# Optimization experiments

Measured on AMD Instinct MI355X. Metric: run time of the kernel, lower is better.

The kernel has to match this reference:

```python
import jax, jax.numpy as jnp
import numpy as np

N, L, D, H = 16384, 10, 256, 2
DH = D // H


def setup_inputs() -> dict:
    key = jax.random.key(0)
    ks = jax.random.split(key, 8)
    messages = jax.random.normal(ks[0], (N, L, D), dtype=jnp.float32)
    timestamps = jnp.sort(jax.random.uniform(ks[1], (N, L), dtype=jnp.float32) * 1000.0, axis=-1)
    # TGN-style time encoder params: w initialized as 1/10^linspace(0,9,D)
    w_time = (1.0 / (10.0 ** jnp.linspace(0.0, 9.0, D))).astype(jnp.float32)
    b_time = jnp.zeros((D,), dtype=jnp.float32)
    w_in = jax.random.normal(ks[2], (3 * D, D), dtype=jnp.float32) * 0.02
    b_in = jnp.zeros((3 * D,), dtype=jnp.float32)
    w_out = jax.random.normal(ks[3], (D, D), dtype=jnp.float32) * 0.02
    b_out = jnp.zeros((D,), dtype=jnp.float32)
    lengths = jax.random.randint(ks[4], (N,), 0, L, dtype=jnp.int32)  # valid = lengths+1 in [1, L]
    return {"messages": messages, "timestamps": timestamps, "w_time": w_time,
            "b_time": b_time, "w_in": w_in, "b_in": b_in, "w_out": w_out,
            "b_out": b_out, "lengths": lengths}


def _attn_aggregate(messages, timestamps, w_time, b_time, w_in, b_in, w_out, b_out, lengths):
    # time deltas relative to most recent message per node (as in the torch loop)
    deltas = timestamps - timestamps[:, -1:]                       # [N, L]
    te = jnp.cos(deltas[..., None] * w_time + b_time)              # [N, L, D] time embeddings

    wq, wk, wv = w_in[:D], w_in[D:2 * D], w_in[2 * D:]
    bq, bk, bv = b_in[:D], b_in[D:2 * D], b_in[2 * D:]
    # query = messages, key = time embeddings, value = messages (MHA over per-node window)
    q = (messages @ wq.T + bq).reshape(N, L, H, DH)
    k = (te @ wk.T + bk).reshape(N, L, H, DH)
    v = (messages @ wv.T + bv).reshape(N, L, H, DH)

    scores = jnp.einsum("nqhd,nkhd->nhqk", q, k) / jnp.sqrt(jnp.float32(DH))  # [N,H,L,L]
    # right-aligned padding: first (L - (lengths+1)) positions are padding
    valid = lengths + 1                                            # [N], in [1, L]
    pos = jnp.arange(L)
    pad = pos[None, :] < (L - valid)[:, None]                      # [N, L] True = pad
    scores = jnp.where(pad[:, None, None, :], jnp.float32(-1e9), scores)
    attn = jax.nn.softmax(scores, axis=-1)
    ctx = jnp.einsum("nhqk,nkhd->nqhd", attn, v).reshape(N, L, D)
    out = ctx @ w_out.T + b_out                                    # [N, L, D]
    return out[:, -1, :]                                           # aggregated message per node [N, D]


def reference(messages, timestamps, w_time, b_time, w_in, b_in, w_out, b_out, lengths):
    return _attn_aggregate(messages, timestamps, w_time, b_time, w_in, b_in, w_out, b_out, lengths)
```

## Files before the change

### kernel.cpp

```cpp
#include <hip/hip_runtime.h>
#include <hip/hip_bf16.h>

#define N_S 16384
#define LL 10
#define DD 256

typedef __bf16 bf16;
typedef __attribute__((ext_vector_type(8))) __bf16 bf16x8_t;
typedef __attribute__((ext_vector_type(4))) __bf16 bf16x4_t;
typedef __attribute__((ext_vector_type(4))) float f32x4_t;

__device__ __forceinline__ float fast_cos(float x) {
    float r = x * 0.15915494309189535f;
    r = r - rintf(r);
    return __builtin_amdgcn_cosf(r);
}

__device__ __forceinline__ float bf2f(unsigned short u) {
    return __uint_as_float((unsigned)u << 16);
}

__global__ __launch_bounds__(256) void k_pre(
    const float* __restrict__ w_in, const float* __restrict__ b_in,
    const float* __restrict__ w_out, const float* __restrict__ b_out,
    bf16* __restrict__ Apk, bf16* __restrict__ Cpk,
    float* __restrict__ u, float* __restrict__ p,
    float* __restrict__ c2, float* __restrict__ dvec)
{
    const int bid = blockIdx.x;
    const int tid = threadIdx.x;
    if (bid < 512) {
        const int g = bid * 256 + tid;
        {
            const int kk = g >> 9;
            const int nn = g & 511;
            const int h = nn >> 8;
            const int j = nn & 255;
            const float* wq = w_in + (size_t)(h * 128) * 256;
            const float* wk = w_in + (size_t)(256 + h * 128) * 256;
            float s = 0.f;
            for (int d = 0; d < 128; ++d)
                s += wq[d * 256 + kk] * wk[d * 256 + j];
            const int lane = (((kk & 31) >> 3) << 4) + (nn & 15);
            const int idx = ((((nn >> 4) * 8 + (kk >> 5)) * 64 + lane) << 3) + (kk & 7);
            Apk[idx] = (bf16)s;
        }
        {
            const int oo = g >> 9;
            const int kk2 = g & 511;
            const int h = kk2 >> 8;
            const int i = kk2 & 255;
            const float* wv = w_in + (size_t)(512 + h * 128) * 256;
            float s = 0.f;
            for (int d = 0; d < 128; ++d)
                s += wv[d * 256 + i] * w_out[oo * 256 + h * 128 + d];
            const int lane = (((kk2 & 31) >> 3) << 4) + (oo & 15);
            const int idx = ((((oo >> 4) * 16 + (kk2 >> 5)) * 64 + lane) << 3) + (kk2 & 7);
            Cpk[idx] = (bf16)s;
        }
    } else {
        for (int j = tid; j < 512; j += 256) {
            const int h = j >> 8; const int jj = j & 255;
            float s = 0.f;
            for (int d = 0; d < 128; ++d)
                s += b_in[h * 128 + d] * w_in[(size_t)(256 + h * 128 + d) * 256 + jj];
            u[j] = s;
        }
        for (int i = tid; i < 512; i += 256) {
            const int h = i >> 8; const int ii = i & 255;
            float s = 0.f;
            for (int d = 0; d < 128; ++d)
                s += w_in[(size_t)(h * 128 + d) * 256 + ii] * b_in[256 + h * 128 + d];
            p[i] = s;
        }
        if (tid < 2) {
            float s = 0.f;
            for (int d = 0; d < 128; ++d)
                s += b_in[tid * 128 + d] * b_in[256 + tid * 128 + d];
            c2[tid] = s;
        }
        if (tid < 256) {
            float s = b_out[tid];
            for (int t = 0; t < 256; ++t)
                s += b_in[512 + t] * w_out[tid * 256 + t];
            dvec[tid] = s;
        }
    }
}

__global__ __launch_bounds__(256) void k_gemm1(
    const float* __restrict__ messages, const bf16* __restrict__ Apk,
    const float* __restrict__ u, bf16* __restrict__ G)
{
    const int lane = threadIdx.x & 63;
    const int wid = threadIdx.x >> 6;
    const int mblk = blockIdx.x;
    const int nblk = blockIdx.y;
    const int m0 = mblk * 128 + wid * 32;
    const int r16 = lane & 15;
    const int q4 = lane >> 4;

    f32x4_t acc[2][4];
    #pragma unroll
    for (int a = 0; a < 2; ++a)
        #pragma unroll
        for (int b = 0; b < 4; ++b)
            acc[a][b] = (f32x4_t)(0.f);

    #pragma unroll
    for (int ks = 0; ks < 8; ++ks) {
        bf16x8_t afr[2];
        #pragma unroll
        for (int mt = 0; mt < 2; ++mt) {
            const int row = m0 + mt * 16 + r16;
            const float* src = messages + (size_t)row * (LL * DD) + (LL - 1) * DD + ks * 32 + q4 * 8;
            f32x4_t lo = *(const f32x4_t*)(src);
            f32x4_t hi = *(const f32x4_t*)(src + 4);
            bf16x8_t a;
            a[0] = (bf16)lo[0]; a[1] = (bf16)lo[1]; a[2] = (bf16)lo[2]; a[3] = (bf16)lo[3];
            a[4] = (bf16)hi[0]; a[5] = (bf16)hi[1]; a[6] = (bf16)hi[2]; a[7] = (bf16)hi[3];
            afr[mt] = a;
        }
        #pragma unroll
        for (int nt = 0; nt < 4; ++nt) {
            const int nblk16 = nblk * 4 + nt;
            bf16x8_t b = *(const bf16x8_t*)(Apk + (((size_t)(nblk16 * 8 + ks) * 64 + lane) << 3));
            #pragma unroll
            for (int mt = 0; mt < 2; ++mt)
                acc[mt][nt] = __builtin_amdgcn_mfma_f32_16x16x32_bf16(afr[mt], b, acc[mt][nt], 0, 0, 0);
        }
    }
    #pragma unroll
    for (int mt = 0; mt < 2; ++mt)
        #pragma unroll
        for (int nt = 0; nt < 4; ++nt) {
            const int col = nblk * 64 + nt * 16 + r16;
            const float ub = u[col];
            #pragma unroll
            for (int r = 0; r < 4; ++r) {
                const int row = m0 + mt * 16 + q4 * 4 + r;
                G[(size_t)row * 512 + col] = (bf16)(acc[mt][nt][r] + ub);
            }
        }
}

__global__ __launch_bounds__(256) void k_attn(
    const float* __restrict__ messages, const float* __restrict__ timestamps,
    const float* __restrict__ w_time, const float* __restrict__ b_time,
    const int* __restrict__ lengths, const float* __restrict__ p,
    const float* __restrict__ c2, bf16* __restrict__ GY)
{
    const int lane = threadIdx.x & 63;
    const int wid = threadIdx.x >> 6;
    const int n = blockIdx.x * 4 + wid;
    const int d0 = lane * 4;

    const unsigned short* Grow = (const unsigned short*)(GY + (size_t)n * 512);
    float g0[4], g1[4];
    {
        ushort4 a = *(const ushort4*)(Grow + d0);
        ushort4 b = *(const ushort4*)(Grow + 256 + d0);
        g0[0] = bf2f(a.x); g0[1] = bf2f(a.y); g0[2] = bf2f(a.z); g0[3] = bf2f(a.w);
        g1[0] = bf2f(b.x); g1[1] = bf2f(b.y); g1[2] = bf2f(b.z); g1[3] = bf2f(b.w);
    }

    float wt[4], bt[4], m9[4];
    *(f32x4_t*)wt = *(const f32x4_t*)(w_time + d0);
    *(f32x4_t*)bt = *(const f32x4_t*)(b_time + d0);
    *(f32x4_t*)m9 = *(const f32x4_t*)(messages + (size_t)n * (LL * DD) + (LL - 1) * DD + d0);

    const float* tsrow = timestamps + n * LL;
    const float tlast = tsrow[LL - 1];
    const int valid = lengths[n] + 1;
    const int lmin = LL - valid;

    float s0a, s0b;
    {
        f32x4_t p0 = *(const f32x4_t*)(p + d0);
        f32x4_t p1 = *(const f32x4_t*)(p + 256 + d0);
        s0a = m9[0] * p0[0] + m9[1] * p0[1] + m9[2] * p0[2] + m9[3] * p0[3];
        s0b = m9[0] * p1[0] + m9[1] * p1[1] + m9[2] * p1[2] + m9[3] * p1[3];
        #pragma unroll
        for (int m = 1; m < 64; m <<= 1) {
            s0a += __shfl_xor(s0a, m);
            s0b += __shfl_xor(s0b, m);
        }
        s0a += c2[0];
        s0b += c2[1];
    }

    const float scale = 0.08838834764831845f;
    float sc0[LL], sc1[LL];
    #pragma unroll
    for (int l = 0; l < LL; ++l) {
        if (l >= lmin) {
            const float delta = tsrow[l] - tlast;
            float pa = 0.f, pb = 0.f;
            #pragma unroll
            for (int j = 0; j < 4; ++j) {
                const float te = fast_cos(delta * wt[j] + bt[j]);
                pa += g0[j] * te;
                pb += g1[j] * te;
            }
            #pragma unroll
            for (int m = 1; m < 64; m <<= 1) {
                pa += __shfl_xor(pa, m);
                pb += __shfl_xor(pb, m);
            }
            sc0[l] = (pa + s0a) * scale;
            sc1[l] = (pb + s0b) * scale;
        } else {
            sc0[l] = -1e30f;
            sc1[l] = -1e30f;
        }
    }

    float mx0 = sc0[0], mx1 = sc1[0];
    #pragma unroll
    for (int l = 1; l < LL; ++l) {
        mx0 = fmaxf(mx0, sc0[l]);
        mx1 = fmaxf(mx1, sc1[l]);
    }
    float w0[LL], w1[LL];
    float den0 = 0.f, den1 = 0.f;
    #pragma unroll
    for (int l = 0; l < LL; ++l) {
        w0[l] = (l >= lmin) ? __expf(sc0[l] - mx0) : 0.f;
        w1[l] = (l >= lmin) ? __expf(sc1[l] - mx1) : 0.f;
        den0 += w0[l];
        den1 += w1[l];
    }
    const float inv0 = 1.f / den0, inv1 = 1.f / den1;

    float y0[4] = {0.f, 0.f, 0.f, 0.f}, y1[4] = {0.f, 0.f, 0.f, 0.f};
    #pragma unroll
    for (int l = 0; l < LL; ++l) {
        if (l >= lmin) {
            float mv[4];
            if (l == LL - 1) {
                mv[0] = m9[0]; mv[1] = m9[1]; mv[2] = m9[2]; mv[3] = m9[3];
            } else {
                *(f32x4_t*)mv = *(const f32x4_t*)(messages + (size_t)n * (LL * DD) + l * DD + d0);
            }
            const float a0 = w0[l] * inv0, a1 = w1[l] * inv1;
            #pragma unroll
            for (int j = 0; j < 4; ++j) {
                y0[j] += a0 * mv[j];
                y1[j] += a1 * mv[j];
            }
        }
    }

    bf16x4_t v0, v1;
    v0[0] = (bf16)y0[0]; v0[1] = (bf16)y0[1]; v0[2] = (bf16)y0[2]; v0[3] = (bf16)y0[3];
    v1[0] = (bf16)y1[0]; v1[1] = (bf16)y1[1]; v1[2] = (bf16)y1[2]; v1[3] = (bf16)y1[3];
    *(bf16x4_t*)(GY + (size_t)n * 512 + d0) = v0;
    *(bf16x4_t*)(GY + (size_t)n * 512 + 256 + d0) = v1;
}

__global__ __launch_bounds__(256) void k_gemm2(
    const bf16* __restrict__ Y, const bf16* __restrict__ Cpk,
    const float* __restrict__ dvec, float* __restrict__ out)
{
    const int lane = threadIdx.x & 63;
    const int wid = threadIdx.x >> 6;
    const int mblk = blockIdx.x;
    const int nblk = blockIdx.y;
    const int m0 = mblk * 128 + wid * 32;
    const int r16 = lane & 15;
    const int q4 = lane >> 4;

    f32x4_t acc[2][4];
    #pragma unroll
    for (int a = 0; a < 2; ++a)
        #pragma unroll
        for (int b = 0; b < 4; ++b)
            acc[a][b] = (f32x4_t)(0.f);

    #pragma unroll
    for (int ks = 0; ks < 16; ++ks) {
        bf16x8_t afr[2];
        #pragma unroll
        for (int mt = 0; mt < 2; ++mt) {
            const int row = m0 + mt * 16 + r16;
            afr[mt] = *(const bf16x8_t*)(Y + (size_t)row * 512 + ks * 32 + q4 * 8);
        }
        #pragma unroll
        for (int nt = 0; nt < 4; ++nt) {
            const int nblk16 = nblk * 4 + nt;
            bf16x8_t b = *(const bf16x8_t*)(Cpk + (((size_t)(nblk16 * 16 + ks) * 64 + lane) << 3));
            #pragma unroll
            for (int mt = 0; mt < 2; ++mt)
                acc[mt][nt] = __builtin_amdgcn_mfma_f32_16x16x32_bf16(afr[mt], b, acc[mt][nt], 0, 0, 0);
        }
    }
    #pragma unroll
    for (int mt = 0; mt < 2; ++mt)
        #pragma unroll
        for (int nt = 0; nt < 4; ++nt) {
            const int col = nblk * 64 + nt * 16 + r16;
            const float db = dvec[col];
            #pragma unroll
            for (int r = 0; r < 4; ++r) {
                const int row = m0 + mt * 16 + q4 * 4 + r;
                out[(size_t)row * 256 + col] = acc[mt][nt][r] + db;
            }
        }
}

extern "C" void kernel_launch(void* const* d_in, const int* in_sizes, int n_in,
                              void* d_out, int out_size, void* d_ws, size_t ws_size,
                              hipStream_t stream) {
    const float* messages   = (const float*)d_in[0];
    const float* timestamps = (const float*)d_in[1];
    const float* w_time     = (const float*)d_in[2];
    const float* b_time     = (const float*)d_in[3];
    const float* w_in       = (const float*)d_in[4];
    const float* b_in       = (const float*)d_in[5];
    const float* w_out      = (const float*)d_in[6];
    const float* b_out      = (const float*)d_in[7];
    const int*   lengths    = (const int*)d_in[8];
    float* out = (float*)d_out;

    char* ws = (char*)d_ws;
    bf16*  Apk  = (bf16*)(ws);
    bf16*  Cpk  = (bf16*)(ws + 262144);
    float* u    = (float*)(ws + 524288);
    float* p    = (float*)(ws + 526336);
    float* c2   = (float*)(ws + 528384);
    float* dvec = (float*)(ws + 528448);
    bf16*  GY   = (bf16*)(ws + 1048576);

    k_pre<<<dim3(513), dim3(256), 0, stream>>>(w_in, b_in, w_out, b_out,
                                               Apk, Cpk, u, p, c2, dvec);
    k_gemm1<<<dim3(128, 8), dim3(256), 0, stream>>>(messages, Apk, u, GY);
    k_attn<<<dim3(4096), dim3(256), 0, stream>>>(messages, timestamps, w_time, b_time,
                                                 lengths, p, c2, GY);
    k_gemm2<<<dim3(128, 4), dim3(256), 0, stream>>>(GY, Cpk, dvec, out);
}
```

Measured before the change: 326.4 us.

## Fuse gemm1, attention and gemm2 into one kernel with LDS staging

Merges the three per-node kernels into one kernel that processes 32 nodes per block. The intermediate G/Y rows stay in shared memory instead of round-tripping through global memory, and two launches go away. The precompute kernel is also split into 1025 blocks so the Apk and Cpk products run in separate blocks, with unrolled inner loops. The trade-off is a grid of only 512 blocks and heavier per-wave register use (16 accumulators), which may reduce occupancy and latency hiding.

```diff
diff --git a/kernel.cpp b/kernel.cpp
--- a/kernel.cpp
+++ b/kernel.cpp
@@ -14,10 +14,6 @@
     float r = x * 0.15915494309189535f;
     r = r - rintf(r);
     return __builtin_amdgcn_cosf(r);
-}
-
-__device__ __forceinline__ float bf2f(unsigned short u) {
-    return __uint_as_float((unsigned)u << 16);
 }
 
 __global__ __launch_bounds__(256) void k_pre(
@@ -31,37 +27,38 @@
     const int tid = threadIdx.x;
     if (bid < 512) {
         const int g = bid * 256 + tid;
-        {
-            const int kk = g >> 9;
-            const int nn = g & 511;
-            const int h = nn >> 8;
-            const int j = nn & 255;
-            const float* wq = w_in + (size_t)(h * 128) * 256;
-            const float* wk = w_in + (size_t)(256 + h * 128) * 256;
-            float s = 0.f;
-            for (int d = 0; d < 128; ++d)
-                s += wq[d * 256 + kk] * wk[d * 256 + j];
-            const int lane = (((kk & 31) >> 3) << 4) + (nn & 15);
-            const int idx = ((((nn >> 4) * 8 + (kk >> 5)) * 64 + lane) << 3) + (kk & 7);
-            Apk[idx] = (bf16)s;
-        }
-        {
-            const int oo = g >> 9;
-            const int kk2 = g & 511;
-            const int h = kk2 >> 8;
-            const int i = kk2 & 255;
-            const float* wv = w_in + (size_t)(512 + h * 128) * 256;
-            float s = 0.f;
-            for (int d = 0; d < 128; ++d)
-                s += wv[d * 256 + i] * w_out[oo * 256 + h * 128 + d];
-            const int lane = (((kk2 & 31) >> 3) << 4) + (oo & 15);
-            const int idx = ((((oo >> 4) * 16 + (kk2 >> 5)) * 64 + lane) << 3) + (kk2 & 7);
-            Cpk[idx] = (bf16)s;
-        }
+        const int kk = g >> 9;
+        const int nn = g & 511;
+        const int h = nn >> 8;
+        const int j = nn & 255;
+        const float* wq = w_in + (size_t)(h * 128) * 256;
+        const float* wk = w_in + (size_t)(256 + h * 128) * 256;
+        float s = 0.f;
+        #pragma unroll 16
+        for (int d = 0; d < 128; ++d)
+            s += wq[d * 256 + kk] * wk[d * 256 + j];
+        const int lane = (((kk & 31) >> 3) << 4) + (nn & 15);
+        const int idx = ((((nn >> 4) * 8 + (kk >> 5)) * 64 + lane) << 3) + (kk & 7);
+        Apk[idx] = (bf16)s;
+    } else if (bid < 1024) {
+        const int g = (bid - 512) * 256 + tid;
+        const int oo = g >> 9;
+        const int kk2 = g & 511;
+        const int h = kk2 >> 8;
+        const int i = kk2 & 255;
+        const float* wv = w_in + (size_t)(512 + h * 128) * 256;
+        float s = 0.f;
+        #pragma unroll 16
+        for (int d = 0; d < 128; ++d)
+            s += wv[d * 256 + i] * w_out[oo * 256 + h * 128 + d];
+        const int lane = (((kk2 & 31) >> 3) << 4) + (oo & 15);
+        const int idx = ((((oo >> 4) * 16 + (kk2 >> 5)) * 64 + lane) << 3) + (kk2 & 7);
+        Cpk[idx] = (bf16)s;
     } else {
         for (int j = tid; j < 512; j += 256) {
             const int h = j >> 8; const int jj = j & 255;
             float s = 0.f;
+            #pragma unroll 16
             for (int d = 0; d < 128; ++d)
                 s += b_in[h * 128 + d] * w_in[(size_t)(256 + h * 128 + d) * 256 + jj];
             u[j] = s;
@@ -69,18 +66,21 @@
         for (int i = tid; i < 512; i += 256) {
             const int h = i >> 8; const int ii = i & 255;
             float s = 0.f;
+            #pragma unroll 16
             for (int d = 0; d < 128; ++d)
                 s += w_in[(size_t)(h * 128 + d) * 256 + ii] * b_in[256 + h * 128 + d];
             p[i] = s;
         }
         if (tid < 2) {
             float s = 0.f;
+            #pragma unroll 16
             for (int d = 0; d < 128; ++d)
                 s += b_in[tid * 128 + d] * b_in[256 + tid * 128 + d];
             c2[tid] = s;
         }
         if (tid < 256) {
             float s = b_out[tid];
+            #pragma unroll 16
             for (int t = 0; t < 256; ++t)
                 s += b_in[512 + t] * w_out[tid * 256 + t];
             dvec[tid] = s;
@@ -88,224 +88,195 @@
     }
 }
 
-__global__ __launch_bounds__(256) void k_gemm1(
-    const float* __restrict__ messages, const bf16* __restrict__ Apk,
-    const float* __restrict__ u, bf16* __restrict__ G)
+__global__ __launch_bounds__(256, 4) void k_fused(
+    const float* __restrict__ messages, const float* __restrict__ timestamps,
+    const float* __restrict__ w_time, const float* __restrict__ b_time,
+    const int* __restrict__ lengths,
+    const bf16* __restrict__ Apk, const bf16* __restrict__ Cpk,
+    const float* __restrict__ u, const float* __restrict__ p,
+    const float* __restrict__ c2, const float* __restrict__ dvec,
+    float* __restrict__ out)
 {
-    const int lane = threadIdx.x & 63;
-    const int wid = threadIdx.x >> 6;
-    const int mblk = blockIdx.x;
-    const int nblk = blockIdx.y;
-    const int m0 = mblk * 128 + wid * 32;
+    __shared__ __align__(16) bf16 Gs[32][520];
+
+    const int tid = threadIdx.x;
+    const int lane = tid & 63;
+    const int wid = tid >> 6;
     const int r16 = lane & 15;
     const int q4 = lane >> 4;
-
-    f32x4_t acc[2][4];
-    #pragma unroll
-    for (int a = 0; a < 2; ++a)
-        #pragma unroll
-        for (int b = 0; b < 4; ++b)
-            acc[a][b] = (f32x4_t)(0.f);
-
-    #pragma unroll
-    for (int ks = 0; ks < 8; ++ks) {
-        bf16x8_t afr[2];
-        #pragma unroll
-        for (int mt = 0; mt < 2; ++mt) {
-            const int row = m0 + mt * 16 + r16;
-            const float* src = messages + (size_t)row * (LL * DD) + (LL - 1) * DD + ks * 32 + q4 * 8;
-            f32x4_t lo = *(const f32x4_t*)(src);
-            f32x4_t hi = *(const f32x4_t*)(src + 4);
+    const int n0 = blockIdx.x * 32;
+
+    {
+        const int wr = wid >> 1;
+        const int wc = wid & 1;
+        f32x4_t acc[16];
+        #pragma unroll
+        for (int nt = 0; nt < 16; ++nt) acc[nt] = (f32x4_t)(0.f);
+
+        const int arow = n0 + wr * 16 + r16;
+        const float* abase = messages + (size_t)arow * (LL * DD) + (LL - 1) * DD + q4 * 8;
+        #pragma unroll
+        for (int ks = 0; ks < 8; ++ks) {
+            f32x4_t lo = *(const f32x4_t*)(abase + ks * 32);
+            f32x4_t hi = *(const f32x4_t*)(abase + ks * 32 + 4);
             bf16x8_t a;
             a[0] = (bf16)lo[0]; a[1] = (bf16)lo[1]; a[2] = (bf16)lo[2]; a[3] = (bf16)lo[3];
             a[4] = (bf16)hi[0]; a[5] = (bf16)hi[1]; a[6] = (bf16)hi[2]; a[7] = (bf16)hi[3];
-            afr[mt] = a;
-        }
-        #pragma unroll
-        for (int nt = 0; nt < 4; ++nt) {
-            const int nblk16 = nblk * 4 + nt;
-            bf16x8_t b = *(const bf16x8_t*)(Apk + (((size_t)(nblk16 * 8 + ks) * 64 + lane) << 3));
-            #pragma unroll
-            for (int mt = 0; mt < 2; ++mt)
-                acc[mt][nt] = __builtin_amdgcn_mfma_f32_16x16x32_bf16(afr[mt], b, acc[mt][nt], 0, 0, 0);
+            #pragma unroll
+            for (int nt = 0; nt < 16; ++nt) {
+                const int nblk16 = wc * 16 + nt;
+                bf16x8_t b = *(const bf16x8_t*)(Apk + (((size_t)(nblk16 * 8 + ks) * 64 + lane) << 3));
+                acc[nt] = __builtin_amdgcn_mfma_f32_16x16x32_bf16(a, b, acc[nt], 0, 0, 0);
+            }
+        }
+        #pragma unroll
+        for (int nt = 0; nt < 16; ++nt) {
+            const int col = wc * 256 + nt * 16 + r16;
+            const float ub = u[col];
+            #pragma unroll
+            for (int r = 0; r < 4; ++r)
+                Gs[wr * 16 + q4 * 4 + r][col] = (bf16)(acc[nt][r] + ub);
         }
     }
-    #pragma unroll
-    for (int mt = 0; mt < 2; ++mt)
-        #pragma unroll
-        for (int nt = 0; nt < 4; ++nt) {
-            const int col = nblk * 64 + nt * 16 + r16;
-            const float ub = u[col];
+    __syncthreads();
+
+    {
+        const int d0 = lane * 4;
+        float wt[4], bt[4], pv0[4], pv1[4];
+        *(f32x4_t*)wt = *(const f32x4_t*)(w_time + d0);
+        *(f32x4_t*)bt = *(const f32x4_t*)(b_time + d0);
+        *(f32x4_t*)pv0 = *(const f32x4_t*)(p + d0);
+        *(f32x4_t*)pv1 = *(const f32x4_t*)(p + 256 + d0);
+        const float c20 = c2[0], c21 = c2[1];
+        const float scale = 0.08838834764831845f;
+
+        #pragma unroll
+        for (int i = 0; i < 8; ++i) {
+            const int s = wid * 8 + i;
+            const int n = n0 + s;
+
+            float g0[4], g1[4];
+            {
+                bf16x4_t ga = *(const bf16x4_t*)(&Gs[s][d0]);
+                bf16x4_t gb = *(const bf16x4_t*)(&Gs[s][256 + d0]);
+                #pragma unroll
+                for (int j = 0; j < 4; ++j) { g0[j] = (float)ga[j]; g1[j] = (float)gb[j]; }
+            }
+            float m9[4];
+            *(f32x4_t*)m9 = *(const f32x4_t*)(messages + (size_t)n * (LL * DD) + (LL - 1) * DD + d0);
+
+            const float* tsrow = timestamps + n * LL;
+            const float tlast = tsrow[LL - 1];
+            const int valid = lengths[n] + 1;
+            const int lmin = LL - valid;
+
+            float s0a = m9[0]*pv0[0] + m9[1]*pv0[1] + m9[2]*pv0[2] + m9[3]*pv0[3];
+            float s0b = m9[0]*pv1[0] + m9[1]*pv1[1] + m9[2]*pv1[2] + m9[3]*pv1[3];
+            #pragma unroll
+            for (int m = 1; m < 64; m <<= 1) {
+                s0a += __shfl_xor(s0a, m);
+                s0b += __shfl_xor(s0b, m);
+            }
+            s0a += c20; s0b += c21;
+
+            float sc0[LL], sc1[LL];
+            #pragma unroll
+            for (int l = 0; l < LL; ++l) {
+                if (l >= lmin) {
+                    const float delta = tsrow[l] - tlast;
+                    float pa = 0.f, pb = 0.f;
+                    #pragma unroll
+                    for (int j = 0; j < 4; ++j) {
+                        const float te = fast_cos(delta * wt[j] + bt[j]);
+                        pa += g0[j] * te;
+                        pb += g1[j] * te;
+                    }
+                    #pragma unroll
+                    for (int m = 1; m < 64; m <<= 1) {
+                        pa += __shfl_xor(pa, m);
+                        pb += __shfl_xor(pb, m);
+                    }
+                    sc0[l] = (pa + s0a) * scale;
+                    sc1[l] = (pb + s0b) * scale;
+                } else {
+                    sc0[l] = -1e30f;
+                    sc1[l] = -1e30f;
+                }
+            }
+
+            float mx0 = sc0[0], mx1 = sc1[0];
+            #pragma unroll
+            for (int l = 1; l < LL; ++l) {
+                mx0 = fmaxf(mx0, sc0[l]);
+                mx1 = fmaxf(mx1, sc1[l]);
+            }
+            float w0[LL], w1[LL];
+            float den0 = 0.f, den1 = 0.f;
+            #pragma unroll
+            for (int l = 0; l < LL; ++l) {
+                w0[l] = (l >= lmin) ? __expf(sc0[l] - mx0) : 0.f;
+                w1[l] = (l >= lmin) ? __expf(sc1[l] - mx1) : 0.f;
+                den0 += w0[l];
+                den1 += w1[l];
+            }
+            const float inv0 = 1.f / den0, inv1 = 1.f / den1;
+
+            float y0[4] = {0.f,0.f,0.f,0.f}, y1[4] = {0.f,0.f,0.f,0.f};
+            #pragma unroll
+            for (int l = 0; l < LL; ++l) {
+                if (l >= lmin) {
+                    float mv[4];
+                    if (l == LL - 1) {
+                        mv[0]=m9[0]; mv[1]=m9[1]; mv[2]=m9[2]; mv[3]=m9[3];
+                    } else {
+                        *(f32x4_t*)mv = *(const f32x4_t*)(messages + (size_t)n * (LL * DD) + l * DD + d0);
+                    }
+                    const float a0 = w0[l] * inv0, a1 = w1[l] * inv1;
+                    #pragma unroll
+                    for (int j = 0; j < 4; ++j) {
+                        y0[j] += a0 * mv[j];
+                        y1[j] += a1 * mv[j];
+                    }
+                }
+            }
+
+            bf16x4_t v0, v1;
+            v0[0]=(bf16)y0[0]; v0[1]=(bf16)y0[1]; v0[2]=(bf16)y0[2]; v0[3]=(bf16)y0[3];
+            v1[0]=(bf16)y1[0]; v1[1]=(bf16)y1[1]; v1[2]=(bf16)y1[2]; v1[3]=(bf16)y1[3];
+            *(bf16x4_t*)(&Gs[s][d0]) = v0;
+            *(bf16x4_t*)(&Gs[s][256 + d0]) = v1;
+        }
+    }
+    __syncthreads();
+
+    {
+        const int wr2 = wid >> 1;
+        const int wc2 = wid & 1;
+        f32x4_t acc2[8];
+        #pragma unroll
+        for (int nt = 0; nt < 8; ++nt) acc2[nt] = (f32x4_t)(0.f);
+
+        #pragma unroll
+        for (int ks = 0; ks < 16; ++ks) {
+            bf16x8_t a = *(const bf16x8_t*)(&Gs[wr2 * 16 + r16][ks * 32 + q4 * 8]);
+            #pragma unroll
+            for (int nt = 0; nt < 8; ++nt) {
+                const int nblk16 = wc2 * 8 + nt;
+                bf16x8_t b = *(const bf16x8_t*)(Cpk + (((size_t)(nblk16 * 16 + ks) * 64 + lane) << 3));
+                acc2[nt] = __builtin_amdgcn_mfma_f32_16x16x32_bf16(a, b, acc2[nt], 0, 0, 0);
+            }
+        }
+        #pragma unroll
+        for (int nt = 0; nt < 8; ++nt) {
+            const int col = wc2 * 128 + nt * 16 + r16;
+            const float db = dvec[col];
             #pragma unroll
             for (int r = 0; r < 4; ++r) {
-                const int row = m0 + mt * 16 + q4 * 4 + r;
-                G[(size_t)row * 512 + col] = (bf16)(acc[mt][nt][r] + ub);
-            }
-        }
-}
-
-__global__ __launch_bounds__(256) void k_attn(
-    const float* __restrict__ messages, const float* __restrict__ timestamps,
-    const float* __restrict__ w_time, const float* __restrict__ b_time,
-    const int* __restrict__ lengths, const float* __restrict__ p,
-    const float* __restrict__ c2, bf16* __restrict__ GY)
-{
-    const int lane = threadIdx.x & 63;
-    const int wid = threadIdx.x >> 6;
-    const int n = blockIdx.x * 4 + wid;
-    const int d0 = lane * 4;
-
-    const unsigned short* Grow = (const unsigned short*)(GY + (size_t)n * 512);
-    float g0[4], g1[4];
-    {
-        ushort4 a = *(const ushort4*)(Grow + d0);
-        ushort4 b = *(const ushort4*)(Grow + 256 + d0);
-        g0[0] = bf2f(a.x); g0[1] = bf2f(a.y); g0[2] = bf2f(a.z); g0[3] = bf2f(a.w);
-        g1[0] = bf2f(b.x); g1[1] = bf2f(b.y); g1[2] = bf2f(b.z); g1[3] = bf2f(b.w);
+                const int row = n0 + wr2 * 16 + q4 * 4 + r;
+                out[(size_t)row * 256 + col] = acc2[nt][r] + db;
+            }
+        }
     }
-
-    float wt[4], bt[4], m9[4];
-    *(f32x4_t*)wt = *(const f32x4_t*)(w_time + d0);
-    *(f32x4_t*)bt = *(const f32x4_t*)(b_time + d0);
-    *(f32x4_t*)m9 = *(const f32x4_t*)(messages + (size_t)n * (LL * DD) + (LL - 1) * DD + d0);
-
-    const float* tsrow = timestamps + n * LL;
-    const float tlast = tsrow[LL - 1];
-    const int valid = lengths[n] + 1;
-    const int lmin = LL - valid;
-
-    float s0a, s0b;
-    {
-        f32x4_t p0 = *(const f32x4_t*)(p + d0);
-        f32x4_t p1 = *(const f32x4_t*)(p + 256 + d0);
-        s0a = m9[0] * p0[0] + m9[1] * p0[1] + m9[2] * p0[2] + m9[3] * p0[3];
-        s0b = m9[0] * p1[0] + m9[1] * p1[1] + m9[2] * p1[2] + m9[3] * p1[3];
-        #pragma unroll
-        for (int m = 1; m < 64; m <<= 1) {
-            s0a += __shfl_xor(s0a, m);
-            s0b += __shfl_xor(s0b, m);
-        }
-        s0a += c2[0];
-        s0b += c2[1];
-    }
-
-    const float scale = 0.08838834764831845f;
-    float sc0[LL], sc1[LL];
-    #pragma unroll
-    for (int l = 0; l < LL; ++l) {
-        if (l >= lmin) {
-            const float delta = tsrow[l] - tlast;
-            float pa = 0.f, pb = 0.f;
-            #pragma unroll
-            for (int j = 0; j < 4; ++j) {
-                const float te = fast_cos(delta * wt[j] + bt[j]);
-                pa += g0[j] * te;
-                pb += g1[j] * te;
-            }
-            #pragma unroll
-            for (int m = 1; m < 64; m <<= 1) {
-                pa += __shfl_xor(pa, m);
-                pb += __shfl_xor(pb, m);
-            }
-            sc0[l] = (pa + s0a) * scale;
-            sc1[l] = (pb + s0b) * scale;
-        } else {
-            sc0[l] = -1e30f;
-            sc1[l] = -1e30f;
-        }
-    }
-
-    float mx0 = sc0[0], mx1 = sc1[0];
-    #pragma unroll
-    for (int l = 1; l < LL; ++l) {
-        mx0 = fmaxf(mx0, sc0[l]);
-        mx1 = fmaxf(mx1, sc1[l]);
-    }
-    float w0[LL], w1[LL];
-    float den0 = 0.f, den1 = 0.f;
-    #pragma unroll
-    for (int l = 0; l < LL; ++l) {
-        w0[l] = (l >= lmin) ? __expf(sc0[l] - mx0) : 0.f;
-        w1[l] = (l >= lmin) ? __expf(sc1[l] - mx1) : 0.f;
-        den0 += w0[l];
-        den1 += w1[l];
-    }
-    const float inv0 = 1.f / den0, inv1 = 1.f / den1;
-
-    float y0[4] = {0.f, 0.f, 0.f, 0.f}, y1[4] = {0.f, 0.f, 0.f, 0.f};
-    #pragma unroll
-    for (int l = 0; l < LL; ++l) {
-        if (l >= lmin) {
-            float mv[4];
-            if (l == LL - 1) {
-                mv[0] = m9[0]; mv[1] = m9[1]; mv[2] = m9[2]; mv[3] = m9[3];
-            } else {
-                *(f32x4_t*)mv = *(const f32x4_t*)(messages + (size_t)n * (LL * DD) + l * DD + d0);
-            }
-            const float a0 = w0[l] * inv0, a1 = w1[l] * inv1;
-            #pragma unroll
-            for (int j = 0; j < 4; ++j) {
-                y0[j] += a0 * mv[j];
-                y1[j] += a1 * mv[j];
-            }
-        }
-    }
-
-    bf16x4_t v0, v1;
-    v0[0] = (bf16)y0[0]; v0[1] = (bf16)y0[1]; v0[2] = (bf16)y0[2]; v0[3] = (bf16)y0[3];
-    v1[0] = (bf16)y1[0]; v1[1] = (bf16)y1[1]; v1[2] = (bf16)y1[2]; v1[3] = (bf16)y1[3];
-    *(bf16x4_t*)(GY + (size_t)n * 512 + d0) = v0;
-    *(bf16x4_t*)(GY + (size_t)n * 512 + 256 + d0) = v1;
-}
-
-__global__ __launch_bounds__(256) void k_gemm2(
-    const bf16* __restrict__ Y, const bf16* __restrict__ Cpk,
-    const float* __restrict__ dvec, float* __restrict__ out)
-{
-    const int lane = threadIdx.x & 63;
-    const int wid = threadIdx.x >> 6;
-    const int mblk = blockIdx.x;
-    const int nblk = blockIdx.y;
-    const int m0 = mblk * 128 + wid * 32;
-    const int r16 = lane & 15;
-    const int q4 = lane >> 4;
-
-    f32x4_t acc[2][4];
-    #pragma unroll
-    for (int a = 0; a < 2; ++a)
-        #pragma unroll
-        for (int b = 0; b < 4; ++b)
-            acc[a][b] = (f32x4_t)(0.f);
-
-    #pragma unroll
-    for (int ks = 0; ks < 16; ++ks) {
-        bf16x8_t afr[2];
-        #pragma unroll
-        for (int mt = 0; mt < 2; ++mt) {
-            const int row = m0 + mt * 16 + r16;
-            afr[mt] = *(const bf16x8_t*)(Y + (size_t)row * 512 + ks * 32 + q4 * 8);
-        }
-        #pragma unroll
-        for (int nt = 0; nt < 4; ++nt) {
-            const int nblk16 = nblk * 4 + nt;
-            bf16x8_t b = *(const bf16x8_t*)(Cpk + (((size_t)(nblk16 * 16 + ks) * 64 + lane) << 3));
-            #pragma unroll
-            for (int mt = 0; mt < 2; ++mt)
-                acc[mt][nt] = __builtin_amdgcn_mfma_f32_16x16x32_bf16(afr[mt], b, acc[mt][nt], 0, 0, 0);
-        }
-    }
-    #pragma unroll
-    for (int mt = 0; mt < 2; ++mt)
-        #pragma unroll
-        for (int nt = 0; nt < 4; ++nt) {
-            const int col = nblk * 64 + nt * 16 + r16;
-            const float db = dvec[col];
-            #pragma unroll
-            for (int r = 0; r < 4; ++r) {
-                const int row = m0 + mt * 16 + q4 * 4 + r;
-                out[(size_t)row * 256 + col] = acc[mt][nt][r] + db;
-            }
-        }
 }
 
 extern "C" void kernel_launch(void* const* d_in, const int* in_sizes, int n_in,
@@ -329,12 +300,9 @@
     float* p    = (float*)(ws + 526336);
     float* c2   = (float*)(ws + 528384);
     float* dvec = (float*)(ws + 528448);
-    bf16*  GY   = (bf16*)(ws + 1048576);
-
-    k_pre<<<dim3(513), dim3(256), 0, stream>>>(w_in, b_in, w_out, b_out,
-                                               Apk, Cpk, u, p, c2, dvec);
-    k_gemm1<<<dim3(128, 8), dim3(256), 0, stream>>>(messages, Apk, u, GY);
-    k_attn<<<dim3(4096), dim3(256), 0, stream>>>(messages, timestamps, w_time, b_time,
-                                                 lengths, p, c2, GY);
-    k_gemm2<<<dim3(128, 4), dim3(256), 0, stream>>>(GY, Cpk, dvec, out);
+
+    k_pre<<<dim3(1025), dim3(256), 0, stream>>>(w_in, b_in, w_out, b_out,
+                                                Apk, Cpk, u, p, c2, dvec);
+    k_fused<<<dim3(512), dim3(256), 0, stream>>>(messages, timestamps, w_time, b_time,
+                                                 lengths, Apk, Cpk, u, p, c2, dvec, out);
 }
```

After: 386.8 us. 18.5% more time.
